# Optimization experiments

Hardware: AMD Instinct MI355X
Metric: run time of the kernel (lower is better)

The kernel has to match this reference:

```python
import jax, jax.numpy as jnp
import numpy as np

NUM_GROUPS = 8
EPS = 1e-5


def setup_inputs() -> dict:
    key = jax.random.key(0)
    k1, k2 = jax.random.split(key)
    N, C, B = 1_500_000, 64, 16
    data = jax.random.normal(k1, (N, C), dtype=jnp.float32)
    batch_id = jnp.sort(jax.random.randint(k2, (N,), 0, B, dtype=jnp.int32))
    weights = jnp.ones((1, C), dtype=jnp.float32)
    bias = jnp.zeros((1, C), dtype=jnp.float32)
    return {"data": data, "weights": weights, "bias": bias,
            "batch_id": batch_id, "batch_size": B}


def _group_broadcast(x, B, G, Cg):
    # reshape (B, C) -> (B, G, Cg), sum over Cg, broadcast back to (B, C)
    s = x.reshape(B, G, Cg).sum(-1, keepdims=True)        # (B, G, 1)
    return jnp.broadcast_to(s, (B, G, Cg)).reshape(B, G * Cg)


def reference(data, weights, bias, batch_id, batch_size):
    N, C = data.shape
    G = NUM_GROUPS
    Cg = C // G
    ones = jnp.ones((N, 1), dtype=data.dtype)
    # per-batch element count, scaled by channels-per-group (matches torch code)
    count = jax.ops.segment_sum(ones, batch_id, num_segments=batch_size) * Cg  # (B, 1)
    norm = 1.0 / (count + EPS)
    # per-(batch, group) mean
    mean = jax.ops.segment_sum(data, batch_id, num_segments=batch_size) * norm  # (B, C)
    mean = _group_broadcast(mean, batch_size, G, Cg)
    out = data - mean[batch_id]
    # per-(batch, group) variance
    var = jax.ops.segment_sum(out * out, batch_id, num_segments=batch_size) * norm
    var = _group_broadcast(var, batch_size, G, Cg)
    inv_std = 1.0 / jnp.sqrt(var + EPS)
    out = out * inv_std[batch_id]
    return out * weights + bias
```

## Files before the change

### kernel.cpp

```cpp
#include <hip/hip_runtime.h>


#define NGROUPS 8
#define CGQ     8
#define NCHAN   64
#define QPR     16
#define NB      16
#define GNEPS   1e-5f

__global__ void ogn_zero(float* __restrict__ ws) {
    int i = blockIdx.x * blockDim.x + threadIdx.x;
    if (i < 272) ws[i] = 0.f;
}

__global__ __launch_bounds__(256) void ogn_pass1(const float4* __restrict__ d4,
        const int* __restrict__ bid, float* __restrict__ ws,
        int nrows, int rows_per_blk) {
    __shared__ float lsum[NB * NGROUPS];
    __shared__ float lsq[NB * NGROUPS];
    __shared__ float lcnt[NB];
    for (int i = threadIdx.x; i < NB * NGROUPS; i += 256) { lsum[i] = 0.f; lsq[i] = 0.f; }
    if (threadIdx.x < NB) lcnt[threadIdx.x] = 0.f;
    __syncthreads();

    const int q = threadIdx.x & (QPR - 1);
    const int g = q >> 1;
    int row1 = rows_per_blk * (blockIdx.x + 1);
    if (row1 > nrows) row1 = nrows;
    int r = rows_per_blk * blockIdx.x + (threadIdx.x >> 4);

    float s = 0.f, ss = 0.f, cn = 0.f;
    int cur = -1;
    for (; r < row1; r += 16) {
        int b = bid[r];
        if (b != cur) {
            if (cur >= 0) {
                atomicAdd(&lsum[cur * NGROUPS + g], s);
                atomicAdd(&lsq[cur * NGROUPS + g], ss);
                if (q == 0) atomicAdd(&lcnt[cur], cn);
            }
            cur = b; s = 0.f; ss = 0.f; cn = 0.f;
        }
        float4 v = d4[(size_t)r * QPR + q];
        s  += (v.x + v.y) + (v.z + v.w);
        ss += (v.x * v.x + v.y * v.y) + (v.z * v.z + v.w * v.w);
        cn += 1.f;
    }
    if (cur >= 0) {
        atomicAdd(&lsum[cur * NGROUPS + g], s);
        atomicAdd(&lsq[cur * NGROUPS + g], ss);
        if (q == 0) atomicAdd(&lcnt[cur], cn);
    }
    __syncthreads();

    for (int i = threadIdx.x; i < NB * NGROUPS; i += 256) {
        float v1 = lsum[i], v2 = lsq[i];
        if (v1 != 0.f) atomicAdd(&ws[i], v1);
        if (v2 != 0.f) atomicAdd(&ws[128 + i], v2);
    }
    if (threadIdx.x < NB) {
        float v = lcnt[threadIdx.x];
        if (v != 0.f) atomicAdd(&ws[256 + threadIdx.x], v);
    }
}

__global__ void ogn_pass2(float* __restrict__ ws) {
    int i = threadIdx.x;
    if (i >= NB * NGROUPS) return;
    int b = i >> 3;
    float cnt  = ws[256 + b] * (float)CGQ;
    float norm = 1.f / (cnt + GNEPS);
    float sum  = ws[i];
    float m    = sum * norm;
    float var  = (ws[128 + i] - 2.f * m * sum + cnt * m * m) * norm;
    ws[272 + i] = m;
    ws[400 + i] = rsqrtf(var + GNEPS);
}

__global__ __launch_bounds__(256) void ogn_pass3(const float4* __restrict__ d4,
        const int* __restrict__ bid, const float4* __restrict__ w4,
        const float4* __restrict__ bia4, const float* __restrict__ ws,
        float4* __restrict__ o4, size_t nq) {
    size_t i = (size_t)blockIdx.x * 256 + threadIdx.x;
    const size_t stride = (size_t)gridDim.x * 256;
    for (; i < nq; i += stride) {
        const int q = (int)(i & (QPR - 1));
        const int g = q >> 1;
        const int b = bid[i >> 4];
        const float m  = ws[272 + b * NGROUPS + g];
        const float is = ws[400 + b * NGROUPS + g];
        float4 v  = d4[i];
        float4 wv = w4[q];
        float4 bv = bia4[q];
        float4 o;
        o.x = (v.x - m) * is * wv.x + bv.x;
        o.y = (v.y - m) * is * wv.y + bv.y;
        o.z = (v.z - m) * is * wv.z + bv.z;
        o.w = (v.w - m) * is * wv.w + bv.w;
        o4[i] = o;
    }
}

extern "C" void kernel_launch(void* const* d_in, const int* in_sizes, int n_in,
                              void* d_out, int out_size, void* d_ws, size_t ws_size,
                              hipStream_t stream) {
    const float* data = (const float*)d_in[0];
    const float* wts  = (const float*)d_in[1];
    const float* bias = (const float*)d_in[2];
    const int*   bid  = (const int*)d_in[3];

    const int N = in_sizes[0] / NCHAN;
    float* ws = (float*)d_ws;

    ogn_zero<<<2, 256, 0, stream>>>(ws);

    const int nblk = 2048;
    const int rpb  = (N + nblk - 1) / nblk;
    ogn_pass1<<<nblk, 256, 0, stream>>>((const float4*)data, bid, ws, N, rpb);

    ogn_pass2<<<1, 128, 0, stream>>>(ws);

    const size_t nq = (size_t)N * QPR;
    int nblk3 = (int)((nq + 255) / 256);
    if (nblk3 > 2048) nblk3 = 2048;
    ogn_pass3<<<nblk3, 256, 0, stream>>>((const float4*)data, bid,
                                         (const float4*)wts, (const float4*)bias,
                                         ws, (float4*)d_out, nq);
}
```

Baseline: 243.9 us.

## Traverse pass3 rows in reverse per pass1 block and use nontemporal stores

Pass3 now uses the same row-block partition as pass1 and walks each block's rows in reverse, so the most recently read data should still be in L2/MALL when it is re-read. Weights and bias are hoisted out of the loop, per-batch mean and inv_std are cached while the batch id is unchanged, and outputs use nontemporal stores to avoid evicting input lines. Reverse order and block-to-CU mapping may not line up with what is actually cached.

New measurement: 218.9 us. 10.3% less time.

```diff
diff --git a/kernel.cpp b/kernel.cpp
--- a/kernel.cpp
+++ b/kernel.cpp
@@ -7,6 +7,8 @@
 #define QPR     16
 #define NB      16
 #define GNEPS   1e-5f
+
+typedef float vfloat4 __attribute__((ext_vector_type(4)));
 
 __global__ void ogn_zero(float* __restrict__ ws) {
     int i = blockIdx.x * blockDim.x + threadIdx.x;
@@ -80,24 +82,32 @@
 __global__ __launch_bounds__(256) void ogn_pass3(const float4* __restrict__ d4,
         const int* __restrict__ bid, const float4* __restrict__ w4,
         const float4* __restrict__ bia4, const float* __restrict__ ws,
-        float4* __restrict__ o4, size_t nq) {
-    size_t i = (size_t)blockIdx.x * 256 + threadIdx.x;
-    const size_t stride = (size_t)gridDim.x * 256;
-    for (; i < nq; i += stride) {
-        const int q = (int)(i & (QPR - 1));
-        const int g = q >> 1;
-        const int b = bid[i >> 4];
-        const float m  = ws[272 + b * NGROUPS + g];
-        const float is = ws[400 + b * NGROUPS + g];
-        float4 v  = d4[i];
-        float4 wv = w4[q];
-        float4 bv = bia4[q];
-        float4 o;
+        float4* __restrict__ o4, int nrows, int rows_per_blk) {
+    const int q = threadIdx.x & (QPR - 1);
+    const int g = q >> 1;
+    const float4 wv = w4[q];
+    const float4 bv = bia4[q];
+
+    const int row0 = rows_per_blk * blockIdx.x;
+    int row1 = row0 + rows_per_blk;
+    if (row1 > nrows) row1 = nrows;
+
+    int cur = -1;
+    float m = 0.f, is = 0.f;
+    for (int r = row1 - 1 - (int)(threadIdx.x >> 4); r >= row0; r -= 16) {
+        int b = bid[r];
+        if (b != cur) {
+            cur = b;
+            m  = ws[272 + b * NGROUPS + g];
+            is = ws[400 + b * NGROUPS + g];
+        }
+        float4 v = d4[(size_t)r * QPR + q];
+        vfloat4 o;
         o.x = (v.x - m) * is * wv.x + bv.x;
         o.y = (v.y - m) * is * wv.y + bv.y;
         o.z = (v.z - m) * is * wv.z + bv.z;
         o.w = (v.w - m) * is * wv.w + bv.w;
-        o4[i] = o;
+        __builtin_nontemporal_store(o, (vfloat4*)&o4[(size_t)r * QPR + q]);
     }
 }
 
@@ -120,10 +130,7 @@
 
     ogn_pass2<<<1, 128, 0, stream>>>(ws);
 
-    const size_t nq = (size_t)N * QPR;
-    int nblk3 = (int)((nq + 255) / 256);
-    if (nblk3 > 2048) nblk3 = 2048;
-    ogn_pass3<<<nblk3, 256, 0, stream>>>((const float4*)data, bid,
-                                         (const float4*)wts, (const float4*)bias,
-                                         ws, (float4*)d_out, nq);
+    ogn_pass3<<<nblk, 256, 0, stream>>>((const float4*)data, bid,
+                                        (const float4*)wts, (const float4*)bias,
+                                        ws, (float4*)d_out, N, rpb);
 }
```
